# Kernel optimization log

Hardware: AMD Instinct MI355X
Metric: run time of the kernel (lower is better)

The kernel has to match this reference:

```python
import jax, jax.numpy as jnp
import numpy as np

N_FULL = 200000  # full-graph nodes
N_SUB = 80000    # subgraph nodes
E = 800000       # subgraph edges
IN = 128         # input feature dim
HD = 128         # hidden dim
LMAX = 5         # max ACT depth


def setup_inputs() -> dict:
    key = jax.random.key(0)
    ks = jax.random.split(key, 12)
    s = lambda i, shape: jax.random.normal(ks[i], shape, jnp.float32) * 0.05
    return dict(
        x_full=jax.random.normal(ks[0], (N_FULL, IN), jnp.float32),
        W_in=s(1, (HD, IN)), b_in=jnp.zeros((HD,), jnp.float32),
        W_l=s(2, (HD, HD)), b_l=jnp.zeros((HD,), jnp.float32),
        W_r=s(3, (HD, HD)),
        W_e1=s(4, (HD, 3 * HD)), b_e1=jnp.zeros((HD,), jnp.float32),
        W_e2=s(5, (1, HD)), b_e2=jnp.zeros((1,), jnp.float32),
        W_h1=s(6, (64, 2 * HD + 1)), b_h1=jnp.zeros((64,), jnp.float32),
        W_h2=s(7, (1, 64)), b_h2=jnp.zeros((1,), jnp.float32),
        subset=jax.random.randint(ks[8], (N_SUB,), 0, N_FULL),
        edge_index=jax.random.randint(ks[9], (2, E), 0, N_SUB),
    )


def reference(x_full, W_in, b_in, W_l, b_l, W_r, W_e1, b_e1, W_e2, b_e2,
              W_h1, b_h1, W_h2, b_h2, subset, edge_index):
    src, dst = edge_index[0], edge_index[1]
    # in-degree for mean aggregation (PyG SAGEConv default aggr='mean')
    deg = jax.ops.segment_sum(jnp.ones((E,), x_full.dtype), dst, num_segments=N_SUB)
    deg = jnp.maximum(deg, 1.0)[:, None]

    def sage_step(Hn):
        agg = jax.ops.segment_sum(Hn[src], dst, num_segments=N_SUB) / deg
        return jax.nn.relu(agg @ W_l.T + b_l + Hn @ W_r.T)

    # input projection of gathered subgraph features
    Hk = x_full[subset] @ W_in.T + b_in
    u_idx, v_idx = 0, 1  # mapping of (u, v) in relabeled subgraph

    alphas, scores = [], []
    p_not = jnp.float32(1.0)
    for depth_k in range(1, LMAX + 1):
        # incremental: one more shared SAGE step == k fresh steps from H0
        Hk = sage_step(Hk)
        h_u, h_v = Hk[u_idx], Hk[v_idx]
        feat = jnp.concatenate([h_u, h_v, h_u * h_v])            # [3*HD]
        score = jax.nn.relu(feat @ W_e1.T + b_e1) @ W_e2.T + b_e2  # [1]
        hin = jnp.concatenate([h_u, h_v, score])                  # [2*HD+1]
        p_halt = jax.nn.sigmoid(jax.nn.relu(hin @ W_h1.T + b_h1) @ W_h2.T + b_h2)[0]
        alphas.append(p_halt * p_not)
        scores.append(score[0])
        p_not = p_not * (1.0 - p_halt)

    alpha = jnp.stack(alphas)
    alpha = alpha / (alpha.sum() + 1e-8)
    scores_v = jnp.stack(scores)
    final_score = (alpha * scores_v).sum()
    depths = jnp.arange(1, LMAX + 1, dtype=jnp.float32)
    expected_depth = (alpha * depths).sum()
    return final_score, expected_depth, alpha
```

## Files before the change

### kernel.cpp

```cpp
#include <hip/hip_runtime.h>
#include <hip/hip_bf16.h>

#define N_FULL 200000
#define N_SUB  80000
#define E_NUM  800000
#define IN_DIM 128
#define HD     128
#define LMAX   5

#define NB_SCAN ((N_SUB + 255) / 256)
#define NB_E (E_NUM / 256)
#define WCOMB_BLKS 128
#define CSR_STRIDE 64


__global__ __launch_bounds__(256) void fill_wcomb(
    const int* __restrict__ esrc, const int* __restrict__ edst,
    int* __restrict__ cnt, int* __restrict__ csr, int* __restrict__ level,
    const float* __restrict__ W_l, const float* __restrict__ W_r,
    const float* __restrict__ W_in, const float* __restrict__ b_in,
    const float* __restrict__ b_l,
    float* __restrict__ Wc1, float* __restrict__ Wc2, float* __restrict__ bc) {
    int b = blockIdx.x;
    int t = threadIdx.x;
    if (b < NB_E) {
        if (b < NB_SCAN) {
            int i = b * 256 + t;
            if (i < N_SUB) level[i] = (i < 2) ? 0 : 7;
        }
        int i = b * 256 + t;
        int d = edst[i];
        int p = atomicAdd(&cnt[d], 1);
        if (p < CSR_STRIDE) csr[d * CSR_STRIDE + p] = esrc[i];
    } else {
        __shared__ float sf[256];
        int f = b - NB_E;
        if (t < 128) sf[t] = W_l[f * 128 + t];
        else sf[t] = W_r[f * 128 + (t - 128)];
        __syncthreads();
        int c = t & 127, p = t >> 7;
        const float* wrow = p ? (sf + 128) : sf;
        float acc = 0.f;
#pragma unroll 8
        for (int j = 0; j < 128; ++j)
            acc = fmaf(wrow[j], W_in[j * 128 + c], acc);
        (p ? Wc2 : Wc1)[f * 128 + c] = acc;
        if (t < 64) {
            float pa = (sf[t] + sf[128 + t]) * b_in[t] +
                       (sf[t + 64] + sf[192 + t]) * b_in[t + 64];
            for (int off = 32; off; off >>= 1) pa += __shfl_down(pa, off);
            if (t == 0) bc[f] = pa + b_l[f];
        }
    }
}


__global__ void bfs_csr(const int* __restrict__ cnt, const int* __restrict__ csr,
                        int* __restrict__ level, int t) {
    int i = blockIdx.x * blockDim.x + threadIdx.x;
    if (i >= N_SUB) return;
    if (level[i] != t) return;
    int beg = i * CSR_STRIDE, end = beg + cnt[i];
    for (int j = beg; j < end; ++j) {
        int u = csr[j];
        if (level[u] > t + 1) level[u] = t + 1;
    }
}


__global__ __launch_bounds__(256) void hist_levels(const int* __restrict__ level,
                                                   int* __restrict__ bhist) {
    __shared__ int h[8];
    int t = threadIdx.x;
    if (t < 8) h[t] = 0;
    __syncthreads();
    int i = blockIdx.x * 256 + t;
    if (i < N_SUB) {
        int l = level[i];
        if (l > 5) l = 6;
        atomicAdd(&h[l], 1);
    }
    __syncthreads();
    if (t < 8) bhist[blockIdx.x * 8 + t] = h[t];
}

__global__ void scan_hist(int* __restrict__ bhist, int* __restrict__ base,
                          int* __restrict__ cum) {
    __shared__ int tot[8];
    int t = threadIdx.x;
    if (t < 8) {
        int acc = 0;
        for (int b = 0; b < NB_SCAN; ++b) {
            int v = bhist[b * 8 + t];
            bhist[b * 8 + t] = acc;
            acc += v;
        }
        tot[t] = acc;
    }
    __syncthreads();
    if (t == 0) {
        int acc = 0;
        for (int l = 0; l <= 5; ++l) {
            base[l] = acc;
            acc += tot[l];
            cum[l] = acc;
        }
    }
}

__global__ __launch_bounds__(256) void emit_order(const int* __restrict__ level,
                                                  const int* __restrict__ bhist,
                                                  const int* __restrict__ base,
                                                  int* __restrict__ order) {
    __shared__ int woff[4][8];
    int t = threadIdx.x;
    int lane = t & 63, wv = t >> 6;
    int i = blockIdx.x * 256 + t;
    int l = 7;
    if (i < N_SUB) {
        l = level[i];
        if (l > 5) l = 6;
    }
    unsigned long long mybal = 0;
#pragma unroll
    for (int q = 0; q < 8; ++q) {
        unsigned long long b = __ballot(l == q);
        if (q == l) mybal = b;
        if (lane == 0) woff[wv][q] = (int)__popcll(b);
    }
    int inrank = (int)__popcll(mybal & ((1ull << lane) - 1ull));
    __syncthreads();
    if (t < 8) {
        int acc = 0;
        for (int w2 = 0; w2 < 4; ++w2) {
            int c = woff[w2][t];
            woff[w2][t] = acc;
            acc += c;
        }
    }
    __syncthreads();
    if (i < N_SUB && l <= 5) {
        int pos = base[l] + bhist[blockIdx.x * 8 + l] + woff[wv][l] + inrank;
        order[pos] = i;
    }
}


__global__ __launch_bounds__(256) void aggregate_list(
    const float* __restrict__ H, float* __restrict__ Out,
    const int* __restrict__ cnt, const int* __restrict__ csr,
    const int* __restrict__ order, const int* __restrict__ cum, int lvl,
    const int* __restrict__ srcmap) {
    int M = cum[lvl];
    int ngroups = (M + 3) >> 2;
    int wid = threadIdx.x >> 6, lane = threadIdx.x & 63;
    for (int g = blockIdx.x; g < ngroups; g += gridDim.x) {
        int ni = g * 4 + wid;
        if (ni >= M) continue;
        int node = order[ni];
        int deg = cnt[node];
        int beg = node * CSR_STRIDE, end = beg + deg;
        float ax = 0.f, ay = 0.f, bx = 0.f, by = 0.f;
        int j = beg;
        for (; j + 1 < end; j += 2) {
            int s0 = csr[j], s1 = csr[j + 1];
            int r0 = srcmap ? srcmap[s0] : s0;
            int r1 = srcmap ? srcmap[s1] : s1;
            float2 v0 = *(const float2*)(H + (size_t)r0 * HD + lane * 2);
            float2 v1 = *(const float2*)(H + (size_t)r1 * HD + lane * 2);
            ax += v0.x; ay += v0.y;
            bx += v1.x; by += v1.y;
        }
        if (j < end) {
            int s0 = csr[j];
            int r0 = srcmap ? srcmap[s0] : s0;
            float2 v0 = *(const float2*)(H + (size_t)r0 * HD + lane * 2);
            ax += v0.x; ay += v0.y;
        }
        float inv = 1.0f / (float)(deg > 1 ? deg : 1);
        *(float2*)(Out + (size_t)node * HD + lane * 2) =
            make_float2((ax + bx) * inv, (ay + by) * inv);
    }
}


__device__ void dev_head(
    const float* __restrict__ H,
    const float* __restrict__ W_e1, const float* __restrict__ b_e1,
    const float* __restrict__ W_e2, const float* __restrict__ b_e2,
    const float* __restrict__ W_h1, const float* __restrict__ b_h1,
    const float* __restrict__ W_h2, const float* __restrict__ b_h2,
    float* __restrict__ head_out, int kidx) {

    __shared__ float feat[384];
    __shared__ float rowo[128];
    __shared__ float sc_sh;
    int t = threadIdx.x, lane = t & 63, wv = t >> 6;

    __syncthreads();
    if (t < 128) {
        float a = H[t], b = H[128 + t];
        feat[t] = a;
        feat[128 + t] = b;
        feat[256 + t] = a * b;
    }
    __syncthreads();

    for (int r = wv; r < 128; r += 4) {
        const float* wr = W_e1 + r * 384;
        float acc = 0.f;
#pragma unroll
        for (int j = 0; j < 6; ++j)
            acc += feat[lane + 64 * j] * wr[lane + 64 * j];
        for (int off = 32; off; off >>= 1) acc += __shfl_down(acc, off);
        if (lane == 0) rowo[r] = fmaxf(acc + b_e1[r], 0.f) * W_e2[r];
    }
    __syncthreads();
    if (wv == 0) {
        float v = rowo[lane] + rowo[lane + 64];
        for (int off = 32; off; off >>= 1) v += __shfl_down(v, off);
        if (lane == 0) sc_sh = v + b_e2[0];
    }
    __syncthreads();
    float score = sc_sh;

    for (int r = wv; r < 64; r += 4) {
        const float* wh = W_h1 + r * 257;
        float acc = 0.f;
#pragma unroll
        for (int j = 0; j < 4; ++j)
            acc += feat[lane + 64 * j] * wh[lane + 64 * j];
        if (lane == 0) acc += score * wh[256];
        for (int off = 32; off; off >>= 1) acc += __shfl_down(acc, off);
        if (lane == 0) rowo[r] = fmaxf(acc + b_h1[r], 0.f) * W_h2[r];
    }
    __syncthreads();
    if (wv == 0) {
        float v = rowo[lane];
        for (int off = 32; off; off >>= 1) v += __shfl_down(v, off);
        if (lane == 0) {
            float p = 1.f / (1.f + expf(-(v + b_h2[0])));
            head_out[kidx * 2 + 0] = score;
            head_out[kidx * 2 + 1] = p;
        }
    }
    __syncthreads();
}


#define GBM 128
#define GBK 32

__global__ __launch_bounds__(256) void gemm_list(
    const float* __restrict__ A1, const float* __restrict__ A2,
    const float* __restrict__ W1, const float* __restrict__ W2,
    const float* __restrict__ bias, float* __restrict__ Out,
    const int* __restrict__ order, const int* __restrict__ gatherA,
    const int* __restrict__ gatherB, const int* __restrict__ cum, int lvl,
    const float* __restrict__ W_e1, const float* __restrict__ b_e1,
    const float* __restrict__ W_e2, const float* __restrict__ b_e2,
    const float* __restrict__ W_h1, const float* __restrict__ b_h1,
    const float* __restrict__ W_h2, const float* __restrict__ b_h2,
    float* __restrict__ head_out, int head_kidx) {

    __shared__ __align__(16) float As[GBK][132];
    __shared__ __align__(16) float Ws[GBK][132];

    int M = cum[lvl];
    int ntiles = (M + GBM - 1) / GBM;
    int tid = threadIdx.x;
    int tx = tid & 15, ty = tid >> 4;
    int r0 = ty * 4;
    int c0 = tx * 4;

    for (int tile = blockIdx.x; tile < ntiles; tile += gridDim.x) {
        int row0 = tile * GBM;

        float acc[2][2][4][4];
#pragma unroll
        for (int p = 0; p < 2; ++p)
#pragma unroll
            for (int q = 0; q < 2; ++q)
#pragma unroll
                for (int i = 0; i < 4; ++i)
#pragma unroll
                    for (int j = 0; j < 4; ++j) acc[p][q][i][j] = 0.f;

        for (int ch = 0; ch < 8; ++ch) {
            const float* Asrc = (ch < 4) ? A1 : A2;
            const float* Wsrc = (ch < 4) ? W1 : W2;
            const int* gmap = (ch < 4) ? gatherA : gatherB;
            int kbase = (ch & 3) * GBK;

#pragma unroll
            for (int it = 0; it < 4; ++it) {
                int idx = tid + it * 256;
                int m = idx & 127, kq = idx >> 7;
                int row = row0 + m;
                float4 v = make_float4(0.f, 0.f, 0.f, 0.f);
                if (row < M) {
                    int nr = order[row];
                    int ar = gmap ? gmap[nr] : nr;
                    v = *(const float4*)(Asrc + (size_t)ar * 128 + kbase + kq * 4);
                }
                As[kq * 4 + 0][m] = v.x;
                As[kq * 4 + 1][m] = v.y;
                As[kq * 4 + 2][m] = v.z;
                As[kq * 4 + 3][m] = v.w;
            }
#pragma unroll
            for (int it = 0; it < 4; ++it) {
                int idx = tid + it * 256;
                int n = idx >> 3, kq = idx & 7;
                float4 v = *(const float4*)(Wsrc + n * 128 + kbase + kq * 4);
                Ws[kq * 4 + 0][n] = v.x;
                Ws[kq * 4 + 1][n] = v.y;
                Ws[kq * 4 + 2][n] = v.z;
                Ws[kq * 4 + 3][n] = v.w;
            }
            __syncthreads();

#pragma unroll
            for (int kk = 0; kk < GBK; ++kk) {
                float4 a0 = *(const float4*)&As[kk][r0];
                float4 a1 = *(const float4*)&As[kk][r0 + 64];
                float4 w0 = *(const float4*)&Ws[kk][c0];
                float4 w1 = *(const float4*)&Ws[kk][c0 + 64];
                float av[2][4] = {{a0.x, a0.y, a0.z, a0.w}, {a1.x, a1.y, a1.z, a1.w}};
                float wv[2][4] = {{w0.x, w0.y, w0.z, w0.w}, {w1.x, w1.y, w1.z, w1.w}};
#pragma unroll
                for (int p = 0; p < 2; ++p)
#pragma unroll
                    for (int q = 0; q < 2; ++q)
#pragma unroll
                        for (int i = 0; i < 4; ++i)
#pragma unroll
                            for (int j = 0; j < 4; ++j)
                                acc[p][q][i][j] = fmaf(av[p][i], wv[q][j], acc[p][q][i][j]);
            }
            __syncthreads();
        }

#pragma unroll
        for (int p = 0; p < 2; ++p) {
#pragma unroll
            for (int i = 0; i < 4; ++i) {
                int row = row0 + p * 64 + r0 + i;
                if (row >= M) continue;
                int nr = order[row];
                float4 o0, o1;
                o0.x = fmaxf(acc[p][0][i][0] + bias[c0 + 0], 0.f);
                o0.y = fmaxf(acc[p][0][i][1] + bias[c0 + 1], 0.f);
                o0.z = fmaxf(acc[p][0][i][2] + bias[c0 + 2], 0.f);
                o0.w = fmaxf(acc[p][0][i][3] + bias[c0 + 3], 0.f);
                o1.x = fmaxf(acc[p][1][i][0] + bias[c0 + 64], 0.f);
                o1.y = fmaxf(acc[p][1][i][1] + bias[c0 + 65], 0.f);
                o1.z = fmaxf(acc[p][1][i][2] + bias[c0 + 66], 0.f);
                o1.w = fmaxf(acc[p][1][i][3] + bias[c0 + 67], 0.f);
                *(float4*)(Out + (size_t)nr * 128 + c0) = o0;
                *(float4*)(Out + (size_t)nr * 128 + c0 + 64) = o1;
            }
        }

        if (tile == 0 && head_kidx >= 0) {
            dev_head(Out, W_e1, b_e1, W_e2, b_e2, W_h1, b_h1, W_h2, b_h2,
                     head_out, head_kidx);
        }
    }
}


__global__ void finalize(const float* __restrict__ head_out, float* __restrict__ out) {
    if (threadIdx.x == 0 && blockIdx.x == 0) {
        float a[LMAX];
        float p_not = 1.f, s = 0.f;
        for (int k = 0; k < LMAX; ++k) {
            float p = head_out[2 * k + 1];
            a[k] = p * p_not;
            p_not *= (1.f - p);
            s += a[k];
        }
        float inv = 1.f / (s + 1e-8f);
        float fs = 0.f, ed = 0.f;
        for (int k = 0; k < LMAX; ++k) {
            float al = a[k] * inv;
            out[2 + k] = al;
            fs += al * head_out[2 * k];
            ed += al * (float)(k + 1);
        }
        out[0] = fs;
        out[1] = ed;
    }
}


extern "C" void kernel_launch(void* const* d_in, const int* in_sizes, int n_in,
                              void* d_out, int out_size, void* d_ws, size_t ws_size,
                              hipStream_t stream) {
    const float* x_full = (const float*)d_in[0];
    const float* W_in  = (const float*)d_in[1];
    const float* b_in  = (const float*)d_in[2];
    const float* W_l   = (const float*)d_in[3];
    const float* b_l   = (const float*)d_in[4];
    const float* W_r   = (const float*)d_in[5];
    const float* W_e1  = (const float*)d_in[6];
    const float* b_e1  = (const float*)d_in[7];
    const float* W_e2  = (const float*)d_in[8];
    const float* b_e2  = (const float*)d_in[9];
    const float* W_h1  = (const float*)d_in[10];
    const float* b_h1  = (const float*)d_in[11];
    const float* W_h2  = (const float*)d_in[12];
    const float* b_h2  = (const float*)d_in[13];
    const int* subset  = (const int*)d_in[14];
    const int* edge    = (const int*)d_in[15];
    const int* esrc = edge;
    const int* edst = edge + E_NUM;

    char* w = (char*)d_ws;
    float* HA = (float*)w;      w += (size_t)N_SUB * HD * 4;
    float* HB = (float*)w;      w += (size_t)N_SUB * HD * 4;
    int* cnt = (int*)w;         w += (size_t)N_SUB * 4;
    int* csr = (int*)w;         w += (size_t)N_SUB * CSR_STRIDE * 4;
    int* level = (int*)w;       w += (size_t)N_SUB * 4;
    int* order = (int*)w;       w += (size_t)N_SUB * 4;
    int* bhist = (int*)w;       w += (size_t)(NB_SCAN + 1) * 8 * 4;
    int* lvlbase = (int*)w;     w += 64;
    int* cum = (int*)w;         w += 64;
    float* Wc1 = (float*)w;     w += 128 * 128 * 4;
    float* Wc2 = (float*)w;     w += 128 * 128 * 4;
    float* bc = (float*)w;      w += 512;
    float* head_out = (float*)w; w += 256;

    hipMemsetAsync(cnt, 0, (size_t)N_SUB * 4, stream);
    fill_wcomb<<<NB_E + WCOMB_BLKS, 256, 0, stream>>>(
        esrc, edst, cnt, csr, level, W_l, W_r, W_in, b_in, b_l, Wc1, Wc2, bc);

    for (int t = 0; t < 4; ++t)
        bfs_csr<<<NB_SCAN, 256, 0, stream>>>(cnt, csr, level, t);

    hist_levels<<<NB_SCAN, 256, 0, stream>>>(level, bhist);
    scan_hist<<<1, 64, 0, stream>>>(bhist, lvlbase, cum);
    emit_order<<<NB_SCAN, 256, 0, stream>>>(level, bhist, lvlbase, order);

    aggregate_list<<<2048, 256, 0, stream>>>(
        x_full, HB, cnt, csr, order, cum, 4, subset);
    gemm_list<<<256, 256, 0, stream>>>(
        HB, x_full, Wc1, Wc2, bc, HA, order, nullptr, subset, cum, 4,
        W_e1, b_e1, W_e2, b_e2, W_h1, b_h1, W_h2, b_h2, head_out, 0);

    aggregate_list<<<64, 256, 0, stream>>>(
        HA, HB, cnt, csr, order, cum, 3, nullptr);
    gemm_list<<<32, 256, 0, stream>>>(
        HB, HA, W_l, W_r, b_l, HA, order, nullptr, nullptr, cum, 3,
        W_e1, b_e1, W_e2, b_e2, W_h1, b_h1, W_h2, b_h2, head_out, 1);

    aggregate_list<<<16, 256, 0, stream>>>(
        HA, HB, cnt, csr, order, cum, 2, nullptr);
    gemm_list<<<2, 256, 0, stream>>>(
        HB, HA, W_l, W_r, b_l, HA, order, nullptr, nullptr, cum, 2,
        W_e1, b_e1, W_e2, b_e2, W_h1, b_h1, W_h2, b_h2, head_out, 2);

    aggregate_list<<<8, 256, 0, stream>>>(
        HA, HB, cnt, csr, order, cum, 1, nullptr);
    gemm_list<<<1, 256, 0, stream>>>(
        HB, HA, W_l, W_r, b_l, HA, order, nullptr, nullptr, cum, 1,
        W_e1, b_e1, W_e2, b_e2, W_h1, b_h1, W_h2, b_h2, head_out, 3);

    aggregate_list<<<1, 256, 0, stream>>>(
        HA, HB, cnt, csr, order, cum, 0, nullptr);
    gemm_list<<<1, 256, 0, stream>>>(
        HB, HA, W_l, W_r, b_l, HA, order, nullptr, nullptr, cum, 0,
        W_e1, b_e1, W_e2, b_e2, W_h1, b_h1, W_h2, b_h2, head_out, 4);

    finalize<<<1, 1, 0, stream>>>(head_out, (float*)d_out);
}
```

Baseline: 517.1 us.

## Replace level-scan BFS with frontier queue BFS and sequential-row first-layer GEMM

The full-array BFS passes and the histogram/scan/emit kernels that built the level order are replaced by a frontier-queue BFS. Each warp expands one frontier node and appends newly discovered nodes to the order list with atomics, and the last block writes the cumulative counts. The first aggregation now writes its results contiguously by order position and records the gathered source row, so a new GEMM reads its A operand sequentially and scatters outputs through the order list. This removes several launches and full-node scans in exchange for atomic contention and a register-prefetched GEMM. Degree is also clamped to the CSR stride when reading neighbours.

```diff
diff --git a/kernel.cpp b/kernel.cpp
--- a/kernel.cpp
+++ b/kernel.cpp
@@ -20,7 +20,8 @@
     const float* __restrict__ W_l, const float* __restrict__ W_r,
     const float* __restrict__ W_in, const float* __restrict__ b_in,
     const float* __restrict__ b_l,
-    float* __restrict__ Wc1, float* __restrict__ Wc2, float* __restrict__ bc) {
+    float* __restrict__ Wc1, float* __restrict__ Wc2, float* __restrict__ bc,
+    int* __restrict__ order, int* __restrict__ cum, int* __restrict__ ctrl) {
     int b = blockIdx.x;
     int t = threadIdx.x;
     if (b < NB_E) {
@@ -33,6 +34,11 @@
         int p = atomicAdd(&cnt[d], 1);
         if (p < CSR_STRIDE) csr[d * CSR_STRIDE + p] = esrc[i];
     } else {
+        if (b == NB_E && t == 0) {
+            order[0] = 0; order[1] = 1;
+            cum[0] = 2;
+            ctrl[0] = 2;
+        }
         __shared__ float sf[256];
         int f = b - NB_E;
         if (t < 128) sf[t] = W_l[f * 128 + t];
@@ -55,93 +61,80 @@
 }
 
 
-__global__ void bfs_csr(const int* __restrict__ cnt, const int* __restrict__ csr,
-                        int* __restrict__ level, int t) {
-    int i = blockIdx.x * blockDim.x + threadIdx.x;
-    if (i >= N_SUB) return;
-    if (level[i] != t) return;
-    int beg = i * CSR_STRIDE, end = beg + cnt[i];
-    for (int j = beg; j < end; ++j) {
-        int u = csr[j];
-        if (level[u] > t + 1) level[u] = t + 1;
-    }
-}
-
-
-__global__ __launch_bounds__(256) void hist_levels(const int* __restrict__ level,
-                                                   int* __restrict__ bhist) {
-    __shared__ int h[8];
-    int t = threadIdx.x;
-    if (t < 8) h[t] = 0;
+__global__ __launch_bounds__(256) void bfs_q(
+    const int* __restrict__ cnt, const int* __restrict__ csr,
+    int* __restrict__ level, int* __restrict__ order,
+    int* __restrict__ cum, int* __restrict__ ctrl, int t) {
+    int fb = (t == 0) ? 0 : cum[t - 1];
+    int fe = cum[t];
+    int lane = threadIdx.x & 63;
+    int gw = blockIdx.x * 4 + (threadIdx.x >> 6);
+    int nw = gridDim.x * 4;
+    for (int fi = fb + gw; fi < fe; fi += nw) {
+        int v = order[fi];
+        int deg = cnt[v];
+        if (deg > CSR_STRIDE) deg = CSR_STRIDE;
+        bool succ = false;
+        int u = -1;
+        if (lane < deg) {
+            u = csr[v * CSR_STRIDE + lane];
+            if (level[u] == 7 && atomicMin(&level[u], t + 1) == 7) succ = true;
+        }
+        unsigned long long m = __ballot(succ);
+        if (m) {
+            int rank = (int)__popcll(m & ((1ull << lane) - 1ull));
+            int leader = __ffsll((long long)m) - 1;
+            int base = 0;
+            if (lane == leader) base = atomicAdd(&ctrl[0], (int)__popcll(m));
+            base = __shfl(base, leader);
+            if (succ) order[base + rank] = u;
+        }
+    }
     __syncthreads();
-    int i = blockIdx.x * 256 + t;
-    if (i < N_SUB) {
-        int l = level[i];
-        if (l > 5) l = 6;
-        atomicAdd(&h[l], 1);
-    }
-    __syncthreads();
-    if (t < 8) bhist[blockIdx.x * 8 + t] = h[t];
-}
-
-__global__ void scan_hist(int* __restrict__ bhist, int* __restrict__ base,
-                          int* __restrict__ cum) {
-    __shared__ int tot[8];
-    int t = threadIdx.x;
-    if (t < 8) {
-        int acc = 0;
-        for (int b = 0; b < NB_SCAN; ++b) {
-            int v = bhist[b * 8 + t];
-            bhist[b * 8 + t] = acc;
-            acc += v;
-        }
-        tot[t] = acc;
-    }
-    __syncthreads();
-    if (t == 0) {
-        int acc = 0;
-        for (int l = 0; l <= 5; ++l) {
-            base[l] = acc;
-            acc += tot[l];
-            cum[l] = acc;
-        }
-    }
-}
-
-__global__ __launch_bounds__(256) void emit_order(const int* __restrict__ level,
-                                                  const int* __restrict__ bhist,
-                                                  const int* __restrict__ base,
-                                                  int* __restrict__ order) {
-    __shared__ int woff[4][8];
-    int t = threadIdx.x;
-    int lane = t & 63, wv = t >> 6;
-    int i = blockIdx.x * 256 + t;
-    int l = 7;
-    if (i < N_SUB) {
-        l = level[i];
-        if (l > 5) l = 6;
-    }
-    unsigned long long mybal = 0;
-#pragma unroll
-    for (int q = 0; q < 8; ++q) {
-        unsigned long long b = __ballot(l == q);
-        if (q == l) mybal = b;
-        if (lane == 0) woff[wv][q] = (int)__popcll(b);
-    }
-    int inrank = (int)__popcll(mybal & ((1ull << lane) - 1ull));
-    __syncthreads();
-    if (t < 8) {
-        int acc = 0;
-        for (int w2 = 0; w2 < 4; ++w2) {
-            int c = woff[w2][t];
-            woff[w2][t] = acc;
-            acc += c;
-        }
-    }
-    __syncthreads();
-    if (i < N_SUB && l <= 5) {
-        int pos = base[l] + bhist[blockIdx.x * 8 + l] + woff[wv][l] + inrank;
-        order[pos] = i;
+    if (threadIdx.x == 0) {
+        __threadfence();
+        if (atomicAdd(&ctrl[1 + t], 1) == (int)gridDim.x - 1)
+            cum[t + 1] = atomicAdd(&ctrl[0], 0);
+    }
+}
+
+
+__global__ __launch_bounds__(256) void aggregate_c4(
+    const float* __restrict__ x_full, float* __restrict__ AGG,
+    int* __restrict__ gsrc,
+    const int* __restrict__ cnt, const int* __restrict__ csr,
+    const int* __restrict__ order, const int* __restrict__ cum,
+    const int* __restrict__ subset) {
+    int M = cum[4];
+    int ngroups = (M + 3) >> 2;
+    int wid = threadIdx.x >> 6, lane = threadIdx.x & 63;
+    for (int g = blockIdx.x; g < ngroups; g += gridDim.x) {
+        int ni = g * 4 + wid;
+        if (ni >= M) continue;
+        int node = order[ni];
+        int deg = cnt[node];
+        int cl = deg > CSR_STRIDE ? CSR_STRIDE : deg;
+        int beg = node * CSR_STRIDE, end = beg + cl;
+        float ax = 0.f, ay = 0.f, bx = 0.f, by = 0.f;
+        int j = beg;
+        for (; j + 1 < end; j += 2) {
+            int r0 = subset[csr[j]];
+            int r1 = subset[csr[j + 1]];
+            float2 v0 = *(const float2*)(x_full + (size_t)r0 * HD + lane * 2);
+            float2 v1 = *(const float2*)(x_full + (size_t)r1 * HD + lane * 2);
+            ax += v0.x; ay += v0.y;
+            bx += v1.x; by += v1.y;
+        }
+        if (j < end) {
+            int r0 = subset[csr[j]];
+            float2 v0 = *(const float2*)(x_full + (size_t)r0 * HD + lane * 2);
+            ax += v0.x; ay += v0.y;
+        }
+        float inv = 1.0f / (float)(deg > 1 ? deg : 1);
+        *(float2*)(AGG + (size_t)ni * HD + lane * 2) =
+            make_float2((ax + bx) * inv, (ay + by) * inv);
+        if (lane == 0 && wid == 0) {  }
+        if (lane == 0) gsrc[ni] = subset[node];
     }
 }
 
@@ -149,8 +142,7 @@
 __global__ __launch_bounds__(256) void aggregate_list(
     const float* __restrict__ H, float* __restrict__ Out,
     const int* __restrict__ cnt, const int* __restrict__ csr,
-    const int* __restrict__ order, const int* __restrict__ cum, int lvl,
-    const int* __restrict__ srcmap) {
+    const int* __restrict__ order, const int* __restrict__ cum, int lvl) {
     int M = cum[lvl];
     int ngroups = (M + 3) >> 2;
     int wid = threadIdx.x >> 6, lane = threadIdx.x & 63;
@@ -159,22 +151,20 @@
         if (ni >= M) continue;
         int node = order[ni];
         int deg = cnt[node];
-        int beg = node * CSR_STRIDE, end = beg + deg;
+        int cl = deg > CSR_STRIDE ? CSR_STRIDE : deg;
+        int beg = node * CSR_STRIDE, end = beg + cl;
         float ax = 0.f, ay = 0.f, bx = 0.f, by = 0.f;
         int j = beg;
         for (; j + 1 < end; j += 2) {
             int s0 = csr[j], s1 = csr[j + 1];
-            int r0 = srcmap ? srcmap[s0] : s0;
-            int r1 = srcmap ? srcmap[s1] : s1;
-            float2 v0 = *(const float2*)(H + (size_t)r0 * HD + lane * 2);
-            float2 v1 = *(const float2*)(H + (size_t)r1 * HD + lane * 2);
+            float2 v0 = *(const float2*)(H + (size_t)s0 * HD + lane * 2);
+            float2 v1 = *(const float2*)(H + (size_t)s1 * HD + lane * 2);
             ax += v0.x; ay += v0.y;
             bx += v1.x; by += v1.y;
         }
         if (j < end) {
             int s0 = csr[j];
-            int r0 = srcmap ? srcmap[s0] : s0;
-            float2 v0 = *(const float2*)(H + (size_t)r0 * HD + lane * 2);
+            float2 v0 = *(const float2*)(H + (size_t)s0 * HD + lane * 2);
             ax += v0.x; ay += v0.y;
         }
         float inv = 1.0f / (float)(deg > 1 ? deg : 1);
@@ -251,12 +241,156 @@
 #define GBM 128
 #define GBK 32
 
+__global__ __launch_bounds__(256) void gemm_seq(
+    const float* __restrict__ AGG, const float* __restrict__ x_full,
+    const int* __restrict__ gsrc,
+    const float* __restrict__ W1, const float* __restrict__ W2,
+    const float* __restrict__ bias, float* __restrict__ HA,
+    const int* __restrict__ order, const int* __restrict__ cum,
+    const float* __restrict__ W_e1, const float* __restrict__ b_e1,
+    const float* __restrict__ W_e2, const float* __restrict__ b_e2,
+    const float* __restrict__ W_h1, const float* __restrict__ b_h1,
+    const float* __restrict__ W_h2, const float* __restrict__ b_h2,
+    float* __restrict__ head_out) {
+
+    __shared__ __align__(16) float As[GBK][132];
+    __shared__ __align__(16) float Ws[GBK][132];
+
+    int M = cum[4];
+    int ntiles = (M + GBM - 1) / GBM;
+    int tid = threadIdx.x;
+    int tx = tid & 15, ty = tid >> 4;
+    int r0 = ty * 4;
+    int c0 = tx * 4;
+
+    for (int tile = blockIdx.x; tile < ntiles; tile += gridDim.x) {
+        int row0 = tile * GBM;
+
+        float acc[2][2][4][4];
+#pragma unroll
+        for (int p = 0; p < 2; ++p)
+#pragma unroll
+            for (int q = 0; q < 2; ++q)
+#pragma unroll
+                for (int i = 0; i < 4; ++i)
+#pragma unroll
+                    for (int j = 0; j < 4; ++j) acc[p][q][i][j] = 0.f;
+
+        float4 ra0, ra1, ra2, ra3, rw0, rw1, rw2, rw3;
+
+#define LOADCH(CH)                                                              \
+        {                                                                       \
+            int ch_ = (CH);                                                     \
+            const float* Wsrc_ = (ch_ < 4) ? W1 : W2;                           \
+            int kbase_ = (ch_ & 3) * GBK;                                       \
+            _Pragma("unroll")                                                   \
+            for (int it = 0; it < 4; ++it) {                                    \
+                int idx = tid + it * 256;                                       \
+                int m = idx & 127, kq = idx >> 7;                               \
+                int row = row0 + m;                                             \
+                float4 v = make_float4(0.f, 0.f, 0.f, 0.f);                     \
+                if (row < M) {                                                  \
+                    if (ch_ < 4)                                                \
+                        v = *(const float4*)(AGG + (size_t)row * 128 + kbase_ + kq * 4); \
+                    else {                                                      \
+                        int ar = gsrc[row];                                     \
+                        v = *(const float4*)(x_full + (size_t)ar * 128 + kbase_ + kq * 4); \
+                    }                                                           \
+                }                                                               \
+                if (it == 0) ra0 = v; else if (it == 1) ra1 = v;                \
+                else if (it == 2) ra2 = v; else ra3 = v;                        \
+            }                                                                   \
+            _Pragma("unroll")                                                   \
+            for (int it = 0; it < 4; ++it) {                                    \
+                int idx = tid + it * 256;                                       \
+                int n = idx >> 3, kq = idx & 7;                                 \
+                float4 v = *(const float4*)(Wsrc_ + n * 128 + kbase_ + kq * 4); \
+                if (it == 0) rw0 = v; else if (it == 1) rw1 = v;                \
+                else if (it == 2) rw2 = v; else rw3 = v;                        \
+            }                                                                   \
+        }
+
+        LOADCH(0);
+        for (int ch = 0; ch < 8; ++ch) {
+            __syncthreads();
+#pragma unroll
+            for (int it = 0; it < 4; ++it) {
+                int idx = tid + it * 256;
+                int m = idx & 127, kq = idx >> 7;
+                float4 v = (it == 0) ? ra0 : (it == 1) ? ra1 : (it == 2) ? ra2 : ra3;
+                As[kq * 4 + 0][m] = v.x;
+                As[kq * 4 + 1][m] = v.y;
+                As[kq * 4 + 2][m] = v.z;
+                As[kq * 4 + 3][m] = v.w;
+            }
+#pragma unroll
+            for (int it = 0; it < 4; ++it) {
+                int idx = tid + it * 256;
+                int n = idx >> 3, kq = idx & 7;
+                float4 v = (it == 0) ? rw0 : (it == 1) ? rw1 : (it == 2) ? rw2 : rw3;
+                Ws[kq * 4 + 0][n] = v.x;
+                Ws[kq * 4 + 1][n] = v.y;
+                Ws[kq * 4 + 2][n] = v.z;
+                Ws[kq * 4 + 3][n] = v.w;
+            }
+            __syncthreads();
+            if (ch < 7) LOADCH(ch + 1);
+
+#pragma unroll
+            for (int kk = 0; kk < GBK; ++kk) {
+                float4 a0 = *(const float4*)&As[kk][r0];
+                float4 a1 = *(const float4*)&As[kk][r0 + 64];
+                float4 w0 = *(const float4*)&Ws[kk][c0];
+                float4 w1 = *(const float4*)&Ws[kk][c0 + 64];
+                float av[2][4] = {{a0.x, a0.y, a0.z, a0.w}, {a1.x, a1.y, a1.z, a1.w}};
+                float wv[2][4] = {{w0.x, w0.y, w0.z, w0.w}, {w1.x, w1.y, w1.z, w1.w}};
+#pragma unroll
+                for (int p = 0; p < 2; ++p)
+#pragma unroll
+                    for (int q = 0; q < 2; ++q)
+#pragma unroll
+                        for (int i = 0; i < 4; ++i)
+#pragma unroll
+                            for (int j = 0; j < 4; ++j)
+                                acc[p][q][i][j] = fmaf(av[p][i], wv[q][j], acc[p][q][i][j]);
+            }
+        }
+#undef LOADCH
+
+#pragma unroll
+        for (int p = 0; p < 2; ++p) {
+#pragma unroll
+            for (int i = 0; i < 4; ++i) {
+                int row = row0 + p * 64 + r0 + i;
+                if (row >= M) continue;
+                int nr = order[row];
+                float4 o0, o1;
+                o0.x = fmaxf(acc[p][0][i][0] + bias[c0 + 0], 0.f);
+                o0.y = fmaxf(acc[p][0][i][1] + bias[c0 + 1], 0.f);
+                o0.z = fmaxf(acc[p][0][i][2] + bias[c0 + 2], 0.f);
+                o0.w = fmaxf(acc[p][0][i][3] + bias[c0 + 3], 0.f);
+                o1.x = fmaxf(acc[p][1][i][0] + bias[c0 + 64], 0.f);
+                o1.y = fmaxf(acc[p][1][i][1] + bias[c0 + 65], 0.f);
+                o1.z = fmaxf(acc[p][1][i][2] + bias[c0 + 66], 0.f);
+                o1.w = fmaxf(acc[p][1][i][3] + bias[c0 + 67], 0.f);
+                *(float4*)(HA + (size_t)nr * 128 + c0) = o0;
+                *(float4*)(HA + (size_t)nr * 128 + c0 + 64) = o1;
+            }
+        }
+
+        if (tile == 0) {
+            dev_head(HA, W_e1, b_e1, W_e2, b_e2, W_h1, b_h1, W_h2, b_h2,
+                     head_out, 0);
+        }
+    }
+}
+
+
 __global__ __launch_bounds__(256) void gemm_list(
     const float* __restrict__ A1, const float* __restrict__ A2,
     const float* __restrict__ W1, const float* __restrict__ W2,
     const float* __restrict__ bias, float* __restrict__ Out,
-    const int* __restrict__ order, const int* __restrict__ gatherA,
-    const int* __restrict__ gatherB, const int* __restrict__ cum, int lvl,
+    const int* __restrict__ order, const int* __restrict__ cum, int lvl,
     const float* __restrict__ W_e1, const float* __restrict__ b_e1,
     const float* __restrict__ W_e2, const float* __restrict__ b_e2,
     const float* __restrict__ W_h1, const float* __restrict__ b_h1,
@@ -289,7 +423,6 @@
         for (int ch = 0; ch < 8; ++ch) {
             const float* Asrc = (ch < 4) ? A1 : A2;
             const float* Wsrc = (ch < 4) ? W1 : W2;
-            const int* gmap = (ch < 4) ? gatherA : gatherB;
             int kbase = (ch & 3) * GBK;
 
 #pragma unroll
@@ -299,8 +432,7 @@
                 int row = row0 + m;
                 float4 v = make_float4(0.f, 0.f, 0.f, 0.f);
                 if (row < M) {
-                    int nr = order[row];
-                    int ar = gmap ? gmap[nr] : nr;
+                    int ar = order[row];
                     v = *(const float4*)(Asrc + (size_t)ar * 128 + kbase + kq * 4);
                 }
                 As[kq * 4 + 0][m] = v.x;
@@ -420,56 +552,49 @@
     float* HA = (float*)w;      w += (size_t)N_SUB * HD * 4;
     float* HB = (float*)w;      w += (size_t)N_SUB * HD * 4;
     int* cnt = (int*)w;         w += (size_t)N_SUB * 4;
+    int* ctrl = (int*)w;        w += 256;
     int* csr = (int*)w;         w += (size_t)N_SUB * CSR_STRIDE * 4;
     int* level = (int*)w;       w += (size_t)N_SUB * 4;
     int* order = (int*)w;       w += (size_t)N_SUB * 4;
-    int* bhist = (int*)w;       w += (size_t)(NB_SCAN + 1) * 8 * 4;
-    int* lvlbase = (int*)w;     w += 64;
+    int* gsrc = (int*)w;        w += (size_t)N_SUB * 4;
     int* cum = (int*)w;         w += 64;
     float* Wc1 = (float*)w;     w += 128 * 128 * 4;
     float* Wc2 = (float*)w;     w += 128 * 128 * 4;
     float* bc = (float*)w;      w += 512;
     float* head_out = (float*)w; w += 256;
 
-    hipMemsetAsync(cnt, 0, (size_t)N_SUB * 4, stream);
+    hipMemsetAsync(cnt, 0, (size_t)N_SUB * 4 + 256, stream);
     fill_wcomb<<<NB_E + WCOMB_BLKS, 256, 0, stream>>>(
-        esrc, edst, cnt, csr, level, W_l, W_r, W_in, b_in, b_l, Wc1, Wc2, bc);
+        esrc, edst, cnt, csr, level, W_l, W_r, W_in, b_in, b_l,
+        Wc1, Wc2, bc, order, cum, ctrl);
 
     for (int t = 0; t < 4; ++t)
-        bfs_csr<<<NB_SCAN, 256, 0, stream>>>(cnt, csr, level, t);
-
-    hist_levels<<<NB_SCAN, 256, 0, stream>>>(level, bhist);
-    scan_hist<<<1, 64, 0, stream>>>(bhist, lvlbase, cum);
-    emit_order<<<NB_SCAN, 256, 0, stream>>>(level, bhist, lvlbase, order);
-
-    aggregate_list<<<2048, 256, 0, stream>>>(
-        x_full, HB, cnt, csr, order, cum, 4, subset);
-    gemm_list<<<256, 256, 0, stream>>>(
-        HB, x_full, Wc1, Wc2, bc, HA, order, nullptr, subset, cum, 4,
-        W_e1, b_e1, W_e2, b_e2, W_h1, b_h1, W_h2, b_h2, head_out, 0);
-
-    aggregate_list<<<64, 256, 0, stream>>>(
-        HA, HB, cnt, csr, order, cum, 3, nullptr);
+        bfs_q<<<32, 256, 0, stream>>>(cnt, csr, level, order, cum, ctrl, t);
+
+    aggregate_c4<<<2048, 256, 0, stream>>>(
+        x_full, HB, gsrc, cnt, csr, order, cum, subset);
+    gemm_seq<<<256, 256, 0, stream>>>(
+        HB, x_full, gsrc, Wc1, Wc2, bc, HA, order, cum,
+        W_e1, b_e1, W_e2, b_e2, W_h1, b_h1, W_h2, b_h2, head_out);
+
+    aggregate_list<<<64, 256, 0, stream>>>(HA, HB, cnt, csr, order, cum, 3);
     gemm_list<<<32, 256, 0, stream>>>(
-        HB, HA, W_l, W_r, b_l, HA, order, nullptr, nullptr, cum, 3,
+        HB, HA, W_l, W_r, b_l, HA, order, cum, 3,
         W_e1, b_e1, W_e2, b_e2, W_h1, b_h1, W_h2, b_h2, head_out, 1);
 
-    aggregate_list<<<16, 256, 0, stream>>>(
-        HA, HB, cnt, csr, order, cum, 2, nullptr);
+    aggregate_list<<<16, 256, 0, stream>>>(HA, HB, cnt, csr, order, cum, 2);
     gemm_list<<<2, 256, 0, stream>>>(
-        HB, HA, W_l, W_r, b_l, HA, order, nullptr, nullptr, cum, 2,
+        HB, HA, W_l, W_r, b_l, HA, order, cum, 2,
         W_e1, b_e1, W_e2, b_e2, W_h1, b_h1, W_h2, b_h2, head_out, 2);
 
-    aggregate_list<<<8, 256, 0, stream>>>(
-        HA, HB, cnt, csr, order, cum, 1, nullptr);
+    aggregate_list<<<8, 256, 0, stream>>>(HA, HB, cnt, csr, order, cum, 1);
     gemm_list<<<1, 256, 0, stream>>>(
-        HB, HA, W_l, W_r, b_l, HA, order, nullptr, nullptr, cum, 1,
+        HB, HA, W_l, W_r, b_l, HA, order, cum, 1,
         W_e1, b_e1, W_e2, b_e2, W_h1, b_h1, W_h2, b_h2, head_out, 3);
 
-    aggregate_list<<<1, 256, 0, stream>>>(
-        HA, HB, cnt, csr, order, cum, 0, nullptr);
+    aggregate_list<<<1, 256, 0, stream>>>(HA, HB, cnt, csr, order, cum, 0);
     gemm_list<<<1, 256, 0, stream>>>(
-        HB, HA, W_l, W_r, b_l, HA, order, nullptr, nullptr, cum, 0,
+        HB, HA, W_l, W_r, b_l, HA, order, cum, 0,
         W_e1, b_e1, W_e2, b_e2, W_h1, b_h1, W_h2, b_h2, head_out, 4);
 
     finalize<<<1, 1, 0, stream>>>(head_out, (float*)d_out);
```

Measured after the change: 487.4 us. 1.06x faster.
